# Optimization experiments

Measured on AMD Instinct MI355X. Metric: run time of the kernel, lower is better.

Reference implementation:

```python
import jax, jax.numpy as jnp
import numpy as np

EMB = 1024; H = 8; HD = EMB // H // 2  # head_dim = 64, q/k use 2*H heads of HD; v uses H heads of 2*HD
FF = 4096; DEPTH = 1
LAM_INIT = float(0.8 - 0.6 * np.exp(-0.3 * DEPTH))

def setup_inputs() -> dict:
    key = jax.random.key(0)
    ks = jax.random.split(key, 12)
    s = lambda k, sh, sc: jax.random.normal(k, sh, jnp.float32) * sc
    return {
        'x': s(ks[0], (2, 2048, EMB), 1.0),
        'ln1_w': jnp.ones((EMB,), jnp.float32), 'ln1_b': jnp.zeros((EMB,), jnp.float32),
        'Wq': s(ks[1], (EMB, EMB), 0.02), 'Wk': s(ks[2], (EMB, EMB), 0.02),
        'Wv': s(ks[3], (EMB, EMB), 0.02), 'Wo': s(ks[4], (EMB, EMB), 0.02),
        'lq1': s(ks[5], (HD,), 0.1), 'lk1': s(ks[6], (HD,), 0.1),
        'lq2': s(ks[7], (HD,), 0.1), 'lk2': s(ks[8], (HD,), 0.1),
        'subln_w': jnp.ones((2 * HD,), jnp.float32),
        'ln2_w': jnp.ones((EMB,), jnp.float32), 'ln2_b': jnp.zeros((EMB,), jnp.float32),
        'W1': s(ks[9], (EMB, FF), 0.02), 'b1': jnp.zeros((FF,), jnp.float32),
        'W2': s(ks[10], (FF, EMB), 0.02), 'b2': jnp.zeros((EMB,), jnp.float32),
    }

def _ln(x, w, b):
    m = jnp.mean(x, -1, keepdims=True)
    v = jnp.var(x, -1, keepdims=True)
    return (x - m) * jax.lax.rsqrt(v + 1e-5) * w + b

def _rms(x, w):
    return x * jax.lax.rsqrt(jnp.mean(x * x, -1, keepdims=True) + 1e-5) * w

def reference(x, ln1_w, ln1_b, Wq, Wk, Wv, Wo, lq1, lk1, lq2, lk2, subln_w, ln2_w, ln2_b, W1, b1, W2, b2):
    B, N, _ = x.shape
    h = _ln(x, ln1_w, ln1_b)
    q = (h @ Wq).reshape(B, N, 2 * H, HD) * (HD ** -0.5)
    k = (h @ Wk).reshape(B, N, 2 * H, HD)
    v = (h @ Wv).reshape(B, N, H, 2 * HD)
    # dual softmax attention maps: [B, 2H, N, N]
    attn = jax.nn.softmax(jnp.einsum('bihd,bjhd->bhij', q, k), axis=-1)
    attn = attn.reshape(B, H, 2, N, N)
    lam = jnp.exp(jnp.sum(lq1 * lk1)) - jnp.exp(jnp.sum(lq2 * lk2)) + LAM_INIT
    a = attn[:, :, 0] - lam * attn[:, :, 1]  # differential attention [B,H,N,N]
    o = jnp.einsum('bhij,bjhd->bihd', a, v)  # [B,N,H,2*HD]
    o = _rms(o, subln_w) * (1.0 - LAM_INIT)
    x = x + o.reshape(B, N, EMB) @ Wo
    h = _ln(x, ln2_w, ln2_b)
    return x + (jax.nn.gelu(h @ W1 + b1, approximate=False) @ W2 + b2)
```

## Files before the change

### kernel.cpp

```cpp
#include <hip/hip_runtime.h>


typedef unsigned short u16;
typedef unsigned int u32;
typedef __attribute__((ext_vector_type(8))) __bf16 bf16x8;
typedef __attribute__((ext_vector_type(4))) float f32x4;
typedef __attribute__((ext_vector_type(4))) u32 u32x4;
typedef __attribute__((ext_vector_type(2))) u32 u32x2;

#define LOG2E 1.4426950408889634f
#define LAM_INIT 0.355509068f
#define ONE_MINUS_LAM_INIT 0.644490932f

__device__ __forceinline__ float bf2f(u16 x) {
  u32 u = ((u32)x) << 16;
  return __builtin_bit_cast(float, u);
}
__device__ __forceinline__ u16 f2bf(float f) {
  u32 u = __builtin_bit_cast(u32, f);
  u32 r = (u + 0x7FFFu + ((u >> 16) & 1u)) >> 16;
  return (u16)r;
}
__device__ __forceinline__ u32 cvtpk(float lo, float hi) {
  u32 r;
  asm("v_cvt_pk_bf16_f32 %0, %1, %2" : "=v"(r) : "v"(lo), "v"(hi));
  return r;
}
__device__ __forceinline__ float fexp2(float x) {
  float r;
  asm("v_exp_f32 %0, %1" : "=v"(r) : "v"(x));
  return r;
}
__device__ __forceinline__ float ldf(const void* p, size_t i, bool f32) {
  return f32 ? ((const float*)p)[i] : bf2f(((const u16*)p)[i]);
}
__device__ __forceinline__ void async16(const u16* g, u16* l) {
  __builtin_amdgcn_global_load_lds((const __attribute__((address_space(1))) u32*)g,
                                   (__attribute__((address_space(3))) u32*)l, 16, 0, 0);
}
__device__ __forceinline__ bf16x8 ld8(const u16* p) { return *(const bf16x8*)p; }

__global__ void detect_kernel(const u32* x, int* flag) {
  int e = (x[threadIdx.x] >> 7) & 0xFF;
  unsigned long long m = __ballot(e >= 90 && e <= 150);
  if (threadIdx.x == 0) flag[0] = (__popcll(m) >= 40) ? 1 : 0;
}

__global__ void lam_kernel(const void* lq1, const void* lk1, const void* lq2,
                           const void* lk2, const int* flag, float* out) {
  const bool f32 = flag[0] == 0;
  int L = threadIdx.x;
  float a = ldf(lq1, L, f32) * ldf(lk1, L, f32);
  float c = ldf(lq2, L, f32) * ldf(lk2, L, f32);
#pragma unroll
  for (int m = 1; m < 64; m <<= 1) { a += __shfl_xor(a, m); c += __shfl_xor(c, m); }
  if (L == 0) out[0] = __expf(a) - __expf(c) + LAM_INIT;
}

__device__ __forceinline__ void unpack8(u32x4 u, float* f) {
#pragma unroll
  for (int i = 0; i < 4; ++i) {
    f[2 * i] = bf2f((u16)(u[i] & 0xffffu));
    f[2 * i + 1] = bf2f((u16)(u[i] >> 16));
  }
}

template <bool XRAW>
__global__ __launch_bounds__(256) void ln_kernel(const void* __restrict__ x,
                                                 const void* __restrict__ w,
                                                 const void* __restrict__ b,
                                                 const int* __restrict__ flag,
                                                 u16* __restrict__ out) {
  const bool f32 = flag[0] == 0;
  const int row = blockIdx.x * 4 + (threadIdx.x >> 6);
  const int L = threadIdx.x & 63;
  float xv[16];
  if (XRAW && f32) {
    const f32x4* xr = (const f32x4*)((const float*)x + (size_t)row * 1024 + L * 16);
#pragma unroll
    for (int i = 0; i < 4; ++i) {
      f32x4 vv = xr[i];
#pragma unroll
      for (int j = 0; j < 4; ++j) xv[i * 4 + j] = vv[j];
    }
  } else {
    const u16* xr = (const u16*)x + (size_t)row * 1024 + L * 16;
    unpack8(*(const u32x4*)xr, xv);
    unpack8(*(const u32x4*)(xr + 8), xv + 8);
  }
  float s = 0.f, sq = 0.f;
#pragma unroll
  for (int i = 0; i < 16; ++i) { s += xv[i]; sq += xv[i] * xv[i]; }
#pragma unroll
  for (int m = 1; m < 64; m <<= 1) { s += __shfl_xor(s, m); sq += __shfl_xor(sq, m); }
  float mean = s * (1.0f / 1024.0f);
  float var = sq * (1.0f / 1024.0f) - mean * mean;
  float rstd = rsqrtf(var + 1e-5f);
  u32 pk[8];
#pragma unroll
  for (int i = 0; i < 8; ++i) {
    float w0 = ldf(w, L * 16 + 2 * i, f32), w1 = ldf(w, L * 16 + 2 * i + 1, f32);
    float b0 = ldf(b, L * 16 + 2 * i, f32), b1v = ldf(b, L * 16 + 2 * i + 1, f32);
    float v0 = (xv[2 * i] - mean) * rstd * w0 + b0;
    float v1 = (xv[2 * i + 1] - mean) * rstd * w1 + b1v;
    pk[i] = (u32)f2bf(v0) | ((u32)f2bf(v1) << 16);
  }
  u32x4 o0 = {pk[0], pk[1], pk[2], pk[3]};
  u32x4 o1 = {pk[4], pk[5], pk[6], pk[7]};
  *(u32x4*)(out + (size_t)row * 1024 + L * 16) = o0;
  *(u32x4*)(out + (size_t)row * 1024 + L * 16 + 8) = o1;
}

__global__ __launch_bounds__(256) void twc_kernel(const void* __restrict__ s0,
                                                  const void* __restrict__ s1,
                                                  const void* __restrict__ s2,
                                                  u16* __restrict__ dst, int sstride,
                                                  int dstride, size_t soff, size_t dzoff,
                                                  const int* __restrict__ flag) {
  __shared__ __align__(16) u16 tile[64][72];
  const bool f32 = flag[0] == 0;
  const void* src = blockIdx.z == 0 ? s0 : (blockIdx.z == 1 ? s1 : s2);
  u16* dz = dst + (size_t)blockIdx.z * dzoff;
  const int r0 = blockIdx.y * 64, c0 = blockIdx.x * 64;
  const int t = threadIdx.x;
  const int rr = t >> 3, cc = t & 7;
#pragma unroll
  for (int i = 0; i < 2; ++i) {
    int row = rr + i * 32;
    size_t idx = (size_t)(r0 + row) * sstride + c0 + cc * 8 + soff;
    if (f32) {
      const f32x4* s = (const f32x4*)((const float*)src + idx);
      f32x4 a = s[0], b = s[1];
      union { u16 t16[8]; u32x4 v; } u_;
#pragma unroll
      for (int j = 0; j < 4; ++j) { u_.t16[j] = f2bf(a[j]); u_.t16[4 + j] = f2bf(b[j]); }
      *(u32x4*)(&tile[row][cc * 8]) = u_.v;
    } else {
      *(u32x4*)(&tile[row][cc * 8]) = *(const u32x4*)((const u16*)src + idx);
    }
  }
  __syncthreads();
  u16* d = dz + (size_t)c0 * dstride + r0;
#pragma unroll
  for (int i = 0; i < 2; ++i) {
    int n = rr + i * 32;
    union { u16 t16[8]; u32x4 v; } u_;
#pragma unroll
    for (int j = 0; j < 8; ++j) u_.t16[j] = tile[cc * 8 + j][n];
    *(u32x4*)(d + (size_t)n * dstride + cc * 8) = u_.v;
  }
}

enum { EP_NONE = 0, EP_RES = 2, EP_GELU = 3, EP_BIASRES = 4, EP_QKV = 5 };

template <int TM, int EPI, bool RESRAW, bool OUTFLEX, bool DB>
__global__ __launch_bounds__(256, 2) void gemm_bt(
    const u16* __restrict__ A, const u16* __restrict__ Bt, void* __restrict__ Cv,
    int M, int N, int K, const void* __restrict__ bias, int boff,
    const void* __restrict__ res, const int* __restrict__ flag,
    u16* __restrict__ kout, u16* __restrict__ vtout) {
  constexpr int MT = TM / 32;
  constexpr int HALF = TM * 64 + 128 * 64;
  extern __shared__ __align__(16) u16 lds[];
  const int t = threadIdx.x;
  const int w = t >> 6, L = t & 63;
  const int quad = L >> 4, l16 = L & 15;
  const int m0 = blockIdx.y * TM, n0 = blockIdx.x * 128;
  const int wm = (TM == 128) ? (w >> 1) * 64 : (w & 1) * 32;
  const int wn = (TM == 128) ? (w & 1) * 64 : (w >> 1) * 64;
  const int srow = L >> 3, spc = L & 7;
  const int sc = spc ^ srow;

  f32x4 acc[MT][4] = {};
  const u16* Ab = A + (size_t)m0 * K;
  const u16* Bb = Bt + (size_t)n0 * K;

  auto stage = [&](int kt, int bsel) {
    u16* base = lds + bsel * HALF;
#pragma unroll
    for (int r = 0; r < TM / 32; ++r) {
      int row = r * 32 + w * 8 + srow;
      async16(Ab + (size_t)row * K + kt + sc * 8, &base[row * 64 + spc * 8]);
    }
#pragma unroll
    for (int r = 0; r < 4; ++r) {
      int row = r * 32 + w * 8 + srow;
      async16(Bb + (size_t)row * K + kt + sc * 8, &base[TM * 64 + row * 64 + spc * 8]);
    }
  };
  auto ktile = [&](const u16* base) {
#pragma unroll
    for (int ks = 0; ks < 2; ++ks) {
      bf16x8 af[MT], bfr[4];
#pragma unroll
      for (int mt = 0; mt < MT; ++mt) {
        int row = wm + mt * 16 + l16;
        af[mt] = ld8(&base[row * 64 + (((ks * 4 + quad) ^ (l16 & 7)) * 8)]);
      }
#pragma unroll
      for (int nt = 0; nt < 4; ++nt) {
        int row = wn + nt * 16 + l16;
        bfr[nt] = ld8(&base[TM * 64 + row * 64 + (((ks * 4 + quad) ^ (l16 & 7)) * 8)]);
      }
#pragma unroll
      for (int mt = 0; mt < MT; ++mt)
#pragma unroll
        for (int nt = 0; nt < 4; ++nt)
          acc[mt][nt] =
              __builtin_amdgcn_mfma_f32_16x16x32_bf16(bfr[nt], af[mt], acc[mt][nt], 0, 0, 0);
    }
  };

  if (DB) {
    const int nst = K >> 6;
    stage(0, 0);
    for (int st = 0; st < nst; ++st) {
      __syncthreads();
      if (st + 1 < nst) stage((st + 1) << 6, (st + 1) & 1);
      ktile(lds + (st & 1) * HALF);
    }
  } else {
    for (int kt = 0; kt < K; kt += 64) {
      stage(kt, 0);
      __syncthreads();
      ktile(lds);
      __syncthreads();
    }
  }

  const bool f32 = flag[0] == 0;
#pragma unroll
  for (int mt = 0; mt < MT; ++mt) {
    const int row = m0 + wm + mt * 16 + l16;
#pragma unroll
    for (int nt = 0; nt < 4; ++nt) {
      const int cb = n0 + wn + nt * 16 + quad * 4;
      float v[4];
#pragma unroll
      for (int r = 0; r < 4; ++r) v[r] = acc[mt][nt][r];

      if (EPI == EP_GELU || EPI == EP_BIASRES) {
        float bv[4];
        if (f32) {
          f32x4 bq = *(const f32x4*)((const float*)bias + boff + cb);
#pragma unroll
          for (int r = 0; r < 4; ++r) bv[r] = bq[r];
        } else {
          u32x2 bq = *(const u32x2*)((const u16*)bias + boff + cb);
          bv[0] = bf2f((u16)(bq[0] & 0xffffu));
          bv[1] = bf2f((u16)(bq[0] >> 16));
          bv[2] = bf2f((u16)(bq[1] & 0xffffu));
          bv[3] = bf2f((u16)(bq[1] >> 16));
        }
        if (EPI == EP_GELU) {
#pragma unroll
          for (int r = 0; r < 4; ++r) {
            float x_ = v[r] + bv[r];
            v[r] = 0.5f * x_ * (1.0f + erff(x_ * 0.70710678118654752f));
          }
        } else {
#pragma unroll
          for (int r = 0; r < 4; ++r) v[r] += bv[r];
        }
      }
      if (EPI == EP_RES || EPI == EP_BIASRES) {
        size_t ri = (size_t)row * N + cb;
        if (RESRAW && f32) {
          f32x4 rq = *(const f32x4*)((const float*)res + ri);
#pragma unroll
          for (int r = 0; r < 4; ++r) v[r] += rq[r];
        } else {
          u32x2 rq = *(const u32x2*)((const u16*)res + ri);
          v[0] += bf2f((u16)(rq[0] & 0xffffu));
          v[1] += bf2f((u16)(rq[0] >> 16));
          v[2] += bf2f((u16)(rq[1] & 0xffffu));
          v[3] += bf2f((u16)(rq[1] >> 16));
        }
      }

      if (EPI == EP_QKV) {
        if (cb < 1024) {
          u32x2 pk2 = {cvtpk(v[0] * 0.125f, v[1] * 0.125f),
                       cvtpk(v[2] * 0.125f, v[3] * 0.125f)};
          *(u32x2*)((u16*)Cv + (size_t)row * 1024 + cb) = pk2;
        } else if (cb < 2048) {
          u32x2 pk2 = {cvtpk(v[0], v[1]), cvtpk(v[2], v[3])};
          *(u32x2*)(kout + (size_t)row * 1024 + (cb - 1024)) = pk2;
        } else {
          int c2 = cb - 2048;
          int bb_ = row >> 11, n = row & 2047, hh = c2 >> 7, d0 = c2 & 127;
#pragma unroll
          for (int r = 0; r < 4; ++r)
            vtout[(size_t)((bb_ * 8 + hh) * 128 + d0 + r) * 2048 + n] = f2bf(v[r]);
        }
      } else {
        size_t ci = (size_t)row * N + cb;
        if (OUTFLEX && f32) {
          f32x4 ov = {v[0], v[1], v[2], v[3]};
          *(f32x4*)((float*)Cv + ci) = ov;
        } else {
          u32x2 pk2 = {cvtpk(v[0], v[1]), cvtpk(v[2], v[3])};
          *(u32x2*)((u16*)Cv + ci) = pk2;
        }
      }
    }
  }
}

__global__ __launch_bounds__(512, 4) void attn_kernel(
    const u16* __restrict__ q, const u16* __restrict__ k, const u16* __restrict__ vT,
    const float* __restrict__ lamp, const void* __restrict__ subw,
    const int* __restrict__ flag, u16* __restrict__ o) {
  extern __shared__ __align__(16) u16 lds[];
  constexpr int VB = 16384;
  const int t = threadIdx.x, w = t >> 6, L = t & 63;
  const int quad = L >> 4, l16 = L & 15;
  const int bid = ((blockIdx.x & 7) << 6) | (blockIdx.x >> 3);
  const int qt = bid & 31, h = (bid >> 5) & 7, b = bid >> 8;
  const int q0 = qt * 64;
  const int comp = w >> 2, rh = (w & 3) * 16;
  const int srow = L >> 3, spc = L & 7, sc = spc ^ srow;
  const u16* vb = vT + (size_t)(b * 8 + h) * (128 * 2048);

  auto stageK = [&](int kt, int bsel) {
#pragma unroll
    for (int r = 0; r < 2; ++r) {
      int row = w * 16 + r * 8 + srow;
      int c_ = row >> 6, key = row & 63;
      async16(k + ((size_t)(b * 2048 + kt + key) * 1024 + (2 * h + c_) * 64 + sc * 8),
              &lds[bsel * 8192 + row * 64 + spc * 8]);
    }
  };
  auto stageV = [&](int kt, int bsel) {
#pragma unroll
    for (int r = 0; r < 2; ++r) {
      int dim = w * 16 + r * 8 + srow;
      async16(vb + (size_t)dim * 2048 + kt + sc * 8,
              &lds[VB + bsel * 8192 + dim * 64 + spc * 8]);
    }
  };

  stageK(0, 0);
  stageV(0, 0);
  bf16x8 qf[2];
#pragma unroll
  for (int ks = 0; ks < 2; ++ks) {
    int row = q0 + rh + l16;
    qf[ks] = ld8(q + (size_t)(b * 2048 + row) * 1024 + (2 * h + comp) * 64 +
                 ks * 32 + quad * 8);
  }

  float mst = 0.f, mstl = 0.f, lst = 0.f;
  f32x4 oacc[8] = {};

  auto tile = [&](int bb) {
    f32x4 s[4] = {};
#pragma unroll
    for (int ks = 0; ks < 2; ++ks) {
      bf16x8 kf[4];
#pragma unroll
      for (int nt = 0; nt < 4; ++nt) {
        int row = nt * 16 + l16;
        kf[nt] = ld8(&lds[bb * 8192 + comp * 4096 + row * 64 +
                          (((ks * 4 + quad) ^ (l16 & 7)) * 8)]);
      }
#pragma unroll
      for (int nt = 0; nt < 4; ++nt)
        s[nt] = __builtin_amdgcn_mfma_f32_16x16x32_bf16(kf[nt], qf[ks], s[nt], 0, 0, 0);
    }

    float p[4][4];
#pragma unroll
    for (int nt = 0; nt < 4; ++nt)
#pragma unroll
      for (int r = 0; r < 4; ++r)
        p[nt][r] = fexp2(__builtin_fmaf(s[nt][r], LOG2E, -mstl));

    float ps = 0.f;
#pragma unroll
    for (int nt = 0; nt < 4; ++nt)
#pragma unroll
      for (int r = 0; r < 4; ++r) ps += p[nt][r];

    if (__ballot(!(ps < 1.0e18f))) {
      float mx = -3.0e38f;
#pragma unroll
      for (int nt = 0; nt < 4; ++nt)
#pragma unroll
        for (int r = 0; r < 4; ++r) mx = fmaxf(mx, s[nt][r]);
      mx = fmaxf(mx, __shfl_xor(mx, 16));
      mx = fmaxf(mx, __shfl_xor(mx, 32));
      float mnew = fmaxf(mst, mx);
      float al = fexp2((mst - mnew) * LOG2E);
      mst = mnew;
      mstl = mnew * LOG2E;
      lst *= al;
      ps = 0.f;
#pragma unroll
      for (int nt = 0; nt < 4; ++nt)
#pragma unroll
        for (int r = 0; r < 4; ++r) {
          p[nt][r] = fexp2(__builtin_fmaf(s[nt][r], LOG2E, -mstl));
          ps += p[nt][r];
        }
#pragma unroll
      for (int nt = 0; nt < 8; ++nt)
#pragma unroll
        for (int r = 0; r < 4; ++r) oacc[nt][r] *= al;
    }

    u32 wreg[4][2];
#pragma unroll
    for (int nt = 0; nt < 4; ++nt) {
      wreg[nt][0] = cvtpk(p[nt][0], p[nt][1]);
      wreg[nt][1] = cvtpk(p[nt][2], p[nt][3]);
    }
    ps += __shfl_xor(ps, 16);
    ps += __shfl_xor(ps, 32);
    lst += ps;

#pragma unroll
    for (int ks = 0; ks < 2; ++ks) {
      u32 a0 = wreg[2 * ks][0], b0 = wreg[2 * ks + 1][0];
      u32 a1 = wreg[2 * ks][1], b1 = wreg[2 * ks + 1][1];
      asm("v_permlane32_swap_b32 %0, %1" : "+v"(a0), "+v"(b0));
      asm("v_permlane16_swap_b32 %0, %1" : "+v"(a0), "+v"(b0));
      asm("v_permlane32_swap_b32 %0, %1" : "+v"(a1), "+v"(b1));
      asm("v_permlane16_swap_b32 %0, %1" : "+v"(a1), "+v"(b1));
      u32x4 pw = {a0, a1, b0, b1};
      bf16x8 pf = __builtin_bit_cast(bf16x8, pw);
#pragma unroll
      for (int nt = 0; nt < 8; ++nt) {
        int dim = nt * 16 + l16;
        bf16x8 vf = ld8(&lds[VB + bb * 8192 + dim * 64 +
                             (((ks * 4 + quad) ^ (l16 & 7)) * 8)]);
        oacc[nt] = __builtin_amdgcn_mfma_f32_16x16x32_bf16(vf, pf, oacc[nt], 0, 0, 0);
      }
    }
  };

  for (int ti = 0; ti < 32; ti += 2) {
    __syncthreads();
    stageK((ti + 1) * 64, 1);
    stageV((ti + 1) * 64, 1);
    tile(0);
    __syncthreads();
    if (ti + 2 < 32) {
      stageK((ti + 2) * 64, 0);
      stageV((ti + 2) * 64, 0);
    }
    tile(1);
  }

  {
    float inv = 1.0f / lst;
#pragma unroll
    for (int nt = 0; nt < 8; ++nt)
#pragma unroll
      for (int r = 0; r < 4; ++r) oacc[nt][r] *= inv;
  }

  __syncthreads();
  float* cb = (float*)lds;
  if (comp == 1) {
    int rowc = rh + l16;
#pragma unroll
    for (int nt = 0; nt < 8; ++nt)
      *(f32x4*)(&cb[rowc * 132 + nt * 16 + quad * 4]) = oacc[nt];
  }
  __syncthreads();
  if (comp == 0) {
    const bool f32 = flag[0] == 0;
    float lam = lamp[0];
    int rowc = rh + l16;
    float dv[8][4];
    float sq = 0.f;
#pragma unroll
    for (int nt = 0; nt < 8; ++nt) {
      f32x4 c2 = *(const f32x4*)(&cb[rowc * 132 + nt * 16 + quad * 4]);
#pragma unroll
      for (int r = 0; r < 4; ++r) {
        float d = oacc[nt][r] - lam * c2[r];
        dv[nt][r] = d;
        sq += d * d;
      }
    }
    sq += __shfl_xor(sq, 16);
    sq += __shfl_xor(sq, 32);
    float rms = rsqrtf(sq * (1.0f / 128.0f) + 1e-5f);
    size_t rowg = (size_t)(b * 2048 + q0 + rowc) * 1024 + h * 128;
#pragma unroll
    for (int nt = 0; nt < 8; ++nt) {
      float v0 = dv[nt][0] * rms * ldf(subw, nt * 16 + quad * 4 + 0, f32) * ONE_MINUS_LAM_INIT;
      float v1 = dv[nt][1] * rms * ldf(subw, nt * 16 + quad * 4 + 1, f32) * ONE_MINUS_LAM_INIT;
      float v2 = dv[nt][2] * rms * ldf(subw, nt * 16 + quad * 4 + 2, f32) * ONE_MINUS_LAM_INIT;
      float v3 = dv[nt][3] * rms * ldf(subw, nt * 16 + quad * 4 + 3, f32) * ONE_MINUS_LAM_INIT;
      u32x2 pk2 = {cvtpk(v0, v1), cvtpk(v2, v3)};
      *(u32x2*)(o + rowg + nt * 16 + quad * 4) = pk2;
    }
  }
}

extern "C" void kernel_launch(void* const* d_in, const int* in_sizes, int n_in,
                              void* d_out, int out_size, void* d_ws, size_t ws_size,
                              hipStream_t stream) {
  (void)in_sizes; (void)n_in; (void)out_size;
  const void* x = d_in[0];
  const void* ln1w = d_in[1];
  const void* ln1b = d_in[2];
  const void* Wq = d_in[3];
  const void* Wk = d_in[4];
  const void* Wv = d_in[5];
  const void* Wo = d_in[6];
  const void* lq1 = d_in[7];
  const void* lk1 = d_in[8];
  const void* lq2 = d_in[9];
  const void* lk2 = d_in[10];
  const void* subw = d_in[11];
  const void* ln2w = d_in[12];
  const void* ln2b = d_in[13];
  const void* W1 = d_in[14];
  const void* b1 = d_in[15];
  const void* W2 = d_in[16];
  const void* b2 = d_in[17];

  char* ws = (char*)d_ws;
  const size_t MB = 1u << 20;
  u16* A = (u16*)ws;
  u16* B = (u16*)(ws + 8 * MB);
  u16* C = (u16*)(ws + 16 * MB);
  u16* D = (u16*)(ws + 24 * MB);
  u16* E = (u16*)(ws + 32 * MB);
  const bool MERGED = ws_size >= 81 * MB;
  u16* gfull = (u16*)(ws + 40 * MB);
  u16* W2Tf = (u16*)(ws + 72 * MB);
  float* lam = (float*)(MERGED ? ws + 80 * MB : ws + 40 * MB);
  int* flag = (int*)((char*)lam + 64);
  u16* W2Th = D + 2097152;

  const int g64_2 = (64 * 64 + 128 * 64) * 2 * 2;
  const int g128_2 = (128 * 64 + 128 * 64) * 2 * 2;

  detect_kernel<<<dim3(1), dim3(64), 0, stream>>>((const u32*)x, flag);
  lam_kernel<<<dim3(1), dim3(64), 0, stream>>>(lq1, lk1, lq2, lk2, flag, lam);
  ln_kernel<true><<<dim3(1024), dim3(256), 0, stream>>>(x, ln1w, ln1b, flag, A);

  twc_kernel<<<dim3(16, 16, 3), dim3(256), 0, stream>>>(Wq, Wk, Wv, E, 1024, 1024, 0,
                                                        1048576, flag);
  gemm_bt<128, EP_QKV, false, false, true><<<dim3(24, 32), dim3(256), g128_2, stream>>>(
      A, E, B, 4096, 3072, 1024, nullptr, 0, nullptr, flag, C, D);

  attn_kernel<<<dim3(512), dim3(512), 65536, stream>>>(B, C, D, lam, subw, flag, A);

  twc_kernel<<<dim3(16, 16, 1), dim3(256), 0, stream>>>(Wo, Wo, Wo, D, 1024, 1024, 0, 0,
                                                        flag);
  gemm_bt<64, EP_RES, true, false, true><<<dim3(8, 64), dim3(256), g64_2, stream>>>(
      A, D, E, 4096, 1024, 1024, nullptr, 0, x, flag, nullptr, nullptr);
  ln_kernel<false><<<dim3(1024), dim3(256), 0, stream>>>(E, ln2w, ln2b, flag, A);

  if (MERGED) {
    twc_kernel<<<dim3(64, 16, 1), dim3(256), 0, stream>>>(W1, W1, W1, D, 4096, 1024, 0,
                                                          0, flag);
    twc_kernel<<<dim3(16, 64, 1), dim3(256), 0, stream>>>(W2, W2, W2, W2Tf, 1024, 4096,
                                                          0, 0, flag);
    gemm_bt<128, EP_GELU, false, false, true><<<dim3(32, 32), dim3(256), g128_2,
                                                stream>>>(
        A, D, gfull, 4096, 4096, 1024, b1, 0, nullptr, flag, nullptr, nullptr);
    gemm_bt<64, EP_BIASRES, false, true, true><<<dim3(8, 64), dim3(256), g64_2,
                                                 stream>>>(
        gfull, W2Tf, d_out, 4096, 1024, 4096, b2, 0, E, flag, nullptr, nullptr);
  } else {
    for (int hh = 0; hh < 2; ++hh) {
      twc_kernel<<<dim3(32, 16, 1), dim3(256), 0, stream>>>(W1, W1, W1, D, 4096, 1024,
                                                            (size_t)hh * 2048, 0, flag);
      twc_kernel<<<dim3(16, 32, 1), dim3(256), 0, stream>>>(
          W2, W2, W2, W2Th, 1024, 2048, (size_t)hh * 2048 * 1024, 0, flag);
      gemm_bt<128, EP_GELU, false, false, true><<<dim3(16, 32), dim3(256), g128_2,
                                                  stream>>>(
          A, D, B, 4096, 2048, 1024, b1, hh * 2048, nullptr, flag, nullptr, nullptr);
      if (hh == 0) {
        gemm_bt<64, EP_BIASRES, false, true, true><<<dim3(8, 64), dim3(256), g64_2,
                                                     stream>>>(
            B, W2Th, d_out, 4096, 1024, 2048, b2, 0, E, flag, nullptr, nullptr);
      } else {
        gemm_bt<64, EP_RES, true, true, true><<<dim3(8, 64), dim3(256), g64_2,
                                                stream>>>(
            B, W2Th, d_out, 4096, 1024, 2048, nullptr, 0, d_out, flag, nullptr,
            nullptr);
      }
    }
  }
}
```

Before: 396.7 us.

## Add 256x256-tile GELU GEMM kernel for the FFN up-projection

Adds a dedicated 512-thread GEMM kernel with 256x256 output tiles, double-buffered 64-wide K stages in 128KB of LDS, and a fused bias+GELU epilogue. It is used for the W1 projection when the merged workspace path is active and the large dynamic LDS attribute can be set. Larger tiles raise arithmetic intensity per byte loaded from global memory and cut the block count from 1024 to 256. The cost is fewer blocks than there are CUs, so not every CU gets a tile, plus heavy register use from the 8x4 accumulator array per wave and low occupancy.

Result: no change. 393.5 us (-0.8%).

```diff
diff --git a/kernel.cpp b/kernel.cpp
--- a/kernel.cpp
+++ b/kernel.cpp
@@ -303,6 +303,95 @@
           *(u32x2*)((u16*)Cv + ci) = pk2;
         }
       }
+    }
+  }
+}
+
+__global__ __launch_bounds__(512, 2) void gemm256_gelu(
+    const u16* __restrict__ A, const u16* __restrict__ Bt, u16* __restrict__ Cv,
+    int M, int N, int K, const void* __restrict__ bias,
+    const int* __restrict__ flag) {
+  constexpr int HALF = 2 * 256 * 64;
+  extern __shared__ __align__(16) u16 lds[];
+  const int t = threadIdx.x;
+  const int w = t >> 6, L = t & 63;
+  const int quad = L >> 4, l16 = L & 15;
+  const int m0 = blockIdx.y * 256, n0 = blockIdx.x * 256;
+  const int wm = (w >> 2) * 128, wn = (w & 3) * 64;
+  const int srow = t >> 3, spc = t & 7;
+  const int sc = spc ^ (srow & 7);
+
+  f32x4 acc[8][4] = {};
+  const u16* Ab = A + (size_t)m0 * K;
+  const u16* Bb = Bt + (size_t)n0 * K;
+
+  auto stage = [&](int kt, int bsel) {
+    u16* base = lds + bsel * HALF;
+#pragma unroll
+    for (int r = 0; r < 4; ++r) {
+      int row = r * 64 + srow;
+      async16(Ab + (size_t)row * K + kt + sc * 8, &base[row * 64 + spc * 8]);
+      async16(Bb + (size_t)row * K + kt + sc * 8, &base[16384 + row * 64 + spc * 8]);
+    }
+  };
+  auto ktile = [&](const u16* base) {
+#pragma unroll
+    for (int ks = 0; ks < 2; ++ks) {
+      bf16x8 af[8], bfr[4];
+#pragma unroll
+      for (int mt = 0; mt < 8; ++mt) {
+        int row = wm + mt * 16 + l16;
+        af[mt] = ld8(&base[row * 64 + (((ks * 4 + quad) ^ (l16 & 7)) * 8)]);
+      }
+#pragma unroll
+      for (int nt = 0; nt < 4; ++nt) {
+        int row = wn + nt * 16 + l16;
+        bfr[nt] = ld8(&base[16384 + row * 64 + (((ks * 4 + quad) ^ (l16 & 7)) * 8)]);
+      }
+#pragma unroll
+      for (int mt = 0; mt < 8; ++mt)
+#pragma unroll
+        for (int nt = 0; nt < 4; ++nt)
+          acc[mt][nt] =
+              __builtin_amdgcn_mfma_f32_16x16x32_bf16(bfr[nt], af[mt], acc[mt][nt], 0, 0, 0);
+    }
+  };
+
+  const int nst = K >> 6;
+  stage(0, 0);
+  for (int st = 0; st < nst; ++st) {
+    __syncthreads();
+    if (st + 1 < nst) stage((st + 1) << 6, (st + 1) & 1);
+    ktile(lds + (st & 1) * HALF);
+  }
+
+  const bool f32 = flag[0] == 0;
+#pragma unroll
+  for (int mt = 0; mt < 8; ++mt) {
+    const int row = m0 + wm + mt * 16 + l16;
+#pragma unroll
+    for (int nt = 0; nt < 4; ++nt) {
+      const int cb = n0 + wn + nt * 16 + quad * 4;
+      float bv[4];
+      if (f32) {
+        f32x4 bq = *(const f32x4*)((const float*)bias + cb);
+#pragma unroll
+        for (int r = 0; r < 4; ++r) bv[r] = bq[r];
+      } else {
+        u32x2 bq = *(const u32x2*)((const u16*)bias + cb);
+        bv[0] = bf2f((u16)(bq[0] & 0xffffu));
+        bv[1] = bf2f((u16)(bq[0] >> 16));
+        bv[2] = bf2f((u16)(bq[1] & 0xffffu));
+        bv[3] = bf2f((u16)(bq[1] >> 16));
+      }
+      float v[4];
+#pragma unroll
+      for (int r = 0; r < 4; ++r) {
+        float x_ = acc[mt][nt][r] + bv[r];
+        v[r] = 0.5f * x_ * (1.0f + erff(x_ * 0.70710678118654752f));
+      }
+      u32x2 pk2 = {cvtpk(v[0], v[1]), cvtpk(v[2], v[3])};
+      *(u32x2*)(Cv + (size_t)row * N + cb) = pk2;
     }
   }
 }
@@ -540,6 +629,16 @@
 
   const int g64_2 = (64 * 64 + 128 * 64) * 2 * 2;
   const int g128_2 = (128 * 64 + 128 * 64) * 2 * 2;
+  const int g256_2 = 2 * 2 * 256 * 64 * 2;
+
+  static bool big_lds_ok = false;
+  static bool big_lds_tried = false;
+  if (!big_lds_tried) {
+    big_lds_tried = true;
+    big_lds_ok = hipFuncSetAttribute((const void*)gemm256_gelu,
+                                     hipFuncAttributeMaxDynamicSharedMemorySize,
+                                     g256_2) == hipSuccess;
+  }
 
   detect_kernel<<<dim3(1), dim3(64), 0, stream>>>((const u32*)x, flag);
   lam_kernel<<<dim3(1), dim3(64), 0, stream>>>(lq1, lk1, lq2, lk2, flag, lam);
@@ -563,9 +662,14 @@
                                                           0, flag);
     twc_kernel<<<dim3(16, 64, 1), dim3(256), 0, stream>>>(W2, W2, W2, W2Tf, 1024, 4096,
                                                           0, 0, flag);
-    gemm_bt<128, EP_GELU, false, false, true><<<dim3(32, 32), dim3(256), g128_2,
-                                                stream>>>(
-        A, D, gfull, 4096, 4096, 1024, b1, 0, nullptr, flag, nullptr, nullptr);
+    if (big_lds_ok) {
+      gemm256_gelu<<<dim3(16, 16), dim3(512), g256_2, stream>>>(
+          A, D, gfull, 4096, 4096, 1024, b1, flag);
+    } else {
+      gemm_bt<128, EP_GELU, false, false, true><<<dim3(32, 32), dim3(256), g128_2,
+                                                  stream>>>(
+          A, D, gfull, 4096, 4096, 1024, b1, 0, nullptr, flag, nullptr, nullptr);
+    }
     gemm_bt<64, EP_BIASRES, false, true, true><<<dim3(8, 64), dim3(256), g64_2,
                                                  stream>>>(
         gfull, W2Tf, d_out, 4096, 1024, 4096, b2, 0, E, flag, nullptr, nullptr);
```
